# Performance work log

Hardware: AMD Instinct MI355X
Metric: run time of the kernel (lower is better)

Reference implementation:

```python
import jax, jax.numpy as jnp
import numpy as np

N_NODES = 100000


def setup_inputs() -> dict:
    key = jax.random.key(0)
    ks = jax.random.split(key, 8)
    E = 1600000
    x = jax.random.normal(ks[0], (N_NODES, 128), dtype=jnp.float32)
    src = jax.random.randint(ks[1], (E,), 0, N_NODES, dtype=jnp.int32)
    dst = jax.random.randint(ks[2], (E,), 0, N_NODES, dtype=jnp.int32)
    s = 1.0 / np.sqrt(128.0)
    w_self = jax.random.normal(ks[3], (5, 128, 128), dtype=jnp.float32) * s
    w_neigh = jax.random.normal(ks[4], (5, 128, 128), dtype=jnp.float32) * s
    b = jnp.zeros((5, 128), dtype=jnp.float32)
    w_self_out = jax.random.normal(ks[5], (128, 47), dtype=jnp.float32) * s
    w_neigh_out = jax.random.normal(ks[6], (128, 47), dtype=jnp.float32) * s
    b_out = jnp.zeros((47,), dtype=jnp.float32)
    return {"x": x, "src": src, "dst": dst, "w_self": w_self, "w_neigh": w_neigh,
            "b": b, "w_self_out": w_self_out, "w_neigh_out": w_neigh_out, "b_out": b_out}


def _mean_agg(h, src, dst, inv_deg):
    # segment-sum of source features into destination nodes, then mean
    summed = jax.ops.segment_sum(h[src], dst, num_segments=N_NODES)  # [N, d]
    return summed * inv_deg[:, None]


def _sage_layer(h, src, dst, inv_deg, ws, wn, bias):
    neigh = _mean_agg(h, src, dst, inv_deg)
    return h @ ws + neigh @ wn + bias


def reference(x, src, dst, w_self, w_neigh, b, w_self_out, w_neigh_out, b_out):
    # in-degree, clamped to 1 for isolated nodes (DGL mean aggregator behavior)
    deg = jax.ops.segment_sum(jnp.ones_like(dst, dtype=x.dtype), dst, num_segments=N_NODES)
    inv_deg = 1.0 / jnp.maximum(deg, 1.0)

    # layer 0: no ReLU after (matches original forward)
    h = _sage_layer(x, src, dst, inv_deg, w_self[0], w_neigh[0], b[0])
    # layers 1..4: SAGEConv + ReLU
    for i in range(1, 5):
        h = _sage_layer(h, src, dst, inv_deg, w_self[i], w_neigh[i], b[i])
        h = jax.nn.relu(h)
    # final layer: 128 -> num_classes, no activation
    h = _sage_layer(h, src, dst, inv_deg, w_self_out, w_neigh_out, b_out)
    return h
```

## Files before the change

kernel.cpp:

```cpp
#include <hip/hip_runtime.h>

typedef float f4 __attribute__((ext_vector_type(4)));
typedef float f32x4 __attribute__((ext_vector_type(4)));
typedef float f2 __attribute__((ext_vector_type(2)));
typedef short s16x8 __attribute__((ext_vector_type(8)));
typedef int i4 __attribute__((ext_vector_type(4)));

#define N_NODES 100000
#define NBUCK 196
#define NB1 256

__device__ inline unsigned short f2bf(float f) {
    unsigned int u = __builtin_bit_cast(unsigned int, f);
    u += 0x7FFFu + ((u >> 16) & 1u);
    return (unsigned short)(u >> 16);
}
__device__ inline float bflo(unsigned int v) { return __builtin_bit_cast(float, v << 16); }
__device__ inline float bfhi(unsigned int v) { return __builtin_bit_cast(float, v & 0xFFFF0000u); }

#define GLDS(gp, lp)                                                            \
    __builtin_amdgcn_global_load_lds(                                           \
        (const __attribute__((address_space(1))) void*)(gp),                    \
        (__attribute__((address_space(3))) void*)(lp), 16, 0, 0)

__device__ inline void acc8(f2& a0, f2& a1, f2& a2, f2& a3, i4 u) {
    f2 t0 = {bflo((unsigned int)u[0]), bfhi((unsigned int)u[0])};
    f2 t1 = {bflo((unsigned int)u[1]), bfhi((unsigned int)u[1])};
    f2 t2 = {bflo((unsigned int)u[2]), bfhi((unsigned int)u[2])};
    f2 t3 = {bflo((unsigned int)u[3]), bfhi((unsigned int)u[3])};
    a0 += t0; a1 += t1; a2 += t2; a3 += t3;
}


__global__ __launch_bounds__(256) void k_hist(const int* __restrict__ dst,
                                              int* __restrict__ histG, int E) {
    __shared__ int h[NBUCK];
    int tid = threadIdx.x;
    for (int i = tid; i < NBUCK; i += 256) h[i] = 0;
    __syncthreads();
    int chunk = (E + NB1 - 1) / NB1;
    int s = blockIdx.x * chunk, eN = min(E, s + chunk);
    for (int i = s + tid; i < eN; i += 256) atomicAdd(&h[dst[i] >> 9], 1);
    __syncthreads();
    for (int i = tid; i < NBUCK; i += 256) histG[i * NB1 + blockIdx.x] = h[i];
}

__global__ __launch_bounds__(1024) void k_scanB(int* __restrict__ histG) {
    __shared__ int ps[1024];
    int t = threadIdx.x;
    int base = t * 49;
    int vals[49];
    int sum = 0;
#pragma unroll
    for (int i = 0; i < 49; ++i) { vals[i] = histG[base + i]; sum += vals[i]; }
    ps[t] = sum;
    __syncthreads();
    for (int off = 1; off < 1024; off <<= 1) {
        int v = (t >= off) ? ps[t - off] : 0;
        __syncthreads();
        ps[t] += v;
        __syncthreads();
    }
    int run = ps[t] - sum;
#pragma unroll
    for (int i = 0; i < 49; ++i) { int v = vals[i]; histG[base + i] = run; run += v; }
}

__global__ __launch_bounds__(256) void k_place(const int* __restrict__ src,
                                               const int* __restrict__ dst,
                                               const int* __restrict__ histG,
                                               unsigned int* __restrict__ ebuf, int E) {
    __shared__ int cur[NBUCK];
    int tid = threadIdx.x;
    for (int i = tid; i < NBUCK; i += 256) cur[i] = histG[i * NB1 + blockIdx.x];
    __syncthreads();
    int chunk = (E + NB1 - 1) / NB1;
    int s = blockIdx.x * chunk, eN = min(E, s + chunk);
    for (int i = s + tid; i < eN; i += 256) {
        int d = dst[i];
        int b = d >> 9;
        int pos = atomicAdd(&cur[b], 1);
        ebuf[pos] = (unsigned int)src[i] | ((unsigned int)(d & 511) << 17);
    }
}

__global__ __launch_bounds__(256) void k_csr(const unsigned int* __restrict__ ebuf,
                                             const int* __restrict__ histG,
                                             int* __restrict__ rp, int* __restrict__ col,
                                             float* __restrict__ invd, int N, int E) {
    __shared__ int ldeg[512];
    __shared__ int lbase[512];
    int b = blockIdx.x, tid = threadIdx.x;
    int base = histG[b * NB1];
    int endB = (b == NBUCK - 1) ? E : histG[(b + 1) * NB1];
    int cnt = endB - base;
    int n0 = b << 9;

    ldeg[tid] = 0;
    ldeg[tid + 256] = 0;
    __syncthreads();
    for (int i = tid; i < cnt; i += 256) atomicAdd(&ldeg[ebuf[base + i] >> 17], 1);
    __syncthreads();

    int a0 = ldeg[tid], a1 = ldeg[tid + 256];
    lbase[tid] = a0;
    lbase[tid + 256] = a1;
    __syncthreads();
    for (int off = 1; off < 512; off <<= 1) {
        int v0 = (tid >= off) ? lbase[tid - off] : 0;
        int v1 = (tid + 256 >= off) ? lbase[tid + 256 - off] : 0;
        __syncthreads();
        lbase[tid] += v0;
        lbase[tid + 256] += v1;
        __syncthreads();
    }
    int e0 = lbase[tid] - a0, e1 = lbase[tid + 256] - a1;
    __syncthreads();
    lbase[tid] = e0;
    lbase[tid + 256] = e1;
    ldeg[tid] = 0;
    ldeg[tid + 256] = 0;
    __syncthreads();

    for (int i = tid; i < cnt; i += 256) {
        unsigned int p = ebuf[base + i];
        int dl = p >> 17;
        int pos = base + lbase[dl] + atomicAdd(&ldeg[dl], 1);
        col[pos] = (int)(p & 0x1FFFFu) << 8;
    }

    int g0 = n0 + tid, g1 = n0 + tid + 256;
    if (g0 < N) { rp[g0] = base + e0; invd[g0] = 1.0f / fmaxf((float)a0, 1.0f); }
    if (g1 < N) { rp[g1] = base + e1; invd[g1] = 1.0f / fmaxf((float)a1, 1.0f); }
    if (b == NBUCK - 1 && tid == 0) rp[N] = E;
    if (b == NBUCK - 1 && tid < 32) col[E + tid] = 0;
}


__global__ void k_cvt(const float* __restrict__ x, unsigned short* __restrict__ xb, int n8) {
    int t = blockIdx.x * 256 + threadIdx.x;
    if (t >= n8) return;
    f4 a = *(const f4*)&x[(size_t)t * 8];
    f4 b = *(const f4*)&x[(size_t)t * 8 + 4];
    s16x8 p;
    p[0] = (short)f2bf(a[0]); p[1] = (short)f2bf(a[1]);
    p[2] = (short)f2bf(a[2]); p[3] = (short)f2bf(a[3]);
    p[4] = (short)f2bf(b[0]); p[5] = (short)f2bf(b[1]);
    p[6] = (short)f2bf(b[2]); p[7] = (short)f2bf(b[3]);
    *(s16x8*)&xb[(size_t)t * 8] = p;
}

__global__ void k_prepw(const float* __restrict__ ws, const float* __restrict__ wn,
                        unsigned short* __restrict__ wp) {
    int t = blockIdx.x * 256 + threadIdx.x;
    if (t >= 5 * 4096) return;
    int l = t & 63, nfg = (t >> 6) & 7, ks = (t >> 9) & 7, lyr = t >> 12;
    int n = nfg * 16 + (l & 15);
    s16x8 p;
#pragma unroll
    for (int j = 0; j < 8; ++j) {
        int k = ks * 32 + (l >> 4) * 8 + j;
        float v = (k < 128) ? ws[((size_t)lyr * 128 + k) * 128 + n]
                            : wn[((size_t)lyr * 128 + (k - 128)) * 128 + n];
        p[j] = (short)f2bf(v);
    }
    *(s16x8*)&wp[(size_t)t * 8] = p;
}

__global__ void k_prepwo(const float* __restrict__ wso, const float* __restrict__ wno,
                         unsigned short* __restrict__ wS, unsigned short* __restrict__ wN,
                         const float* __restrict__ bo, float* __restrict__ bo48) {
    int t = blockIdx.x * 256 + threadIdx.x;
    if (t < 48) bo48[t] = (t < 47) ? bo[t] : 0.f;
    if (t >= 2 * 768) return;
    int tbl = t / 768, r = t % 768;
    int ks = r / 192, nf = (r / 64) % 3, l = r & 63;
    int n = nf * 16 + (l & 15);
    const float* W = tbl ? wno : wso;
    unsigned short* dstp = tbl ? wN : wS;
    s16x8 p;
#pragma unroll
    for (int j = 0; j < 8; ++j) {
        int k = ks * 32 + (l >> 4) * 8 + j;
        float v = (n < 47) ? W[(size_t)k * 47 + n] : 0.f;
        p[j] = (short)f2bf(v);
    }
    *(s16x8*)&dstp[(size_t)r * 8] = p;
}


__global__ __launch_bounds__(256) void k_agg(const unsigned short* __restrict__ h,
                                             const int* __restrict__ rp,
                                             const int* __restrict__ col,
                                             const float* __restrict__ invd,
                                             unsigned short* __restrict__ out, int n) {
    int gw = (blockIdx.x * 256 + threadIdx.x) >> 6;
    int lane = threadIdx.x & 63;
    if (gw >= n) return;
    const char* hb = (const char*)h;
    const int sub = lane >> 4;
    const int lb = (lane & 15) * 16;
    int beg = rp[gw], end = rp[gw + 1];
    f2 a0 = {0.f, 0.f}, a1 = {0.f, 0.f}, a2 = {0.f, 0.f}, a3 = {0.f, 0.f};
    int e = beg;
    for (; e + 16 <= end; e += 16) {
        unsigned int c0 = (unsigned int)col[e + sub];
        unsigned int c1 = (unsigned int)col[e + 4 + sub];
        unsigned int c2 = (unsigned int)col[e + 8 + sub];
        unsigned int c3 = (unsigned int)col[e + 12 + sub];
        i4 u0, u1, u2, u3;
        __builtin_memcpy(&u0, hb + c0 + lb, 16);
        __builtin_memcpy(&u1, hb + c1 + lb, 16);
        __builtin_memcpy(&u2, hb + c2 + lb, 16);
        __builtin_memcpy(&u3, hb + c3 + lb, 16);
        acc8(a0, a1, a2, a3, u0);
        acc8(a0, a1, a2, a3, u1);
        acc8(a0, a1, a2, a3, u2);
        acc8(a0, a1, a2, a3, u3);
    }
    if (e + 8 <= end) {
        unsigned int c0 = (unsigned int)col[e + sub];
        unsigned int c1 = (unsigned int)col[e + 4 + sub];
        i4 u0, u1;
        __builtin_memcpy(&u0, hb + c0 + lb, 16);
        __builtin_memcpy(&u1, hb + c1 + lb, 16);
        acc8(a0, a1, a2, a3, u0);
        acc8(a0, a1, a2, a3, u1);
        e += 8;
    }
    if (e < end) {
        unsigned int c0 = (unsigned int)col[e + sub];
        unsigned int c1 = (unsigned int)col[e + 4 + sub];
        i4 u0, u1;
        __builtin_memcpy(&u0, hb + c0 + lb, 16);
        __builtin_memcpy(&u1, hb + c1 + lb, 16);
        if (e + sub < end) acc8(a0, a1, a2, a3, u0);
        if (e + 4 + sub < end) acc8(a0, a1, a2, a3, u1);
    }
#pragma unroll
    for (int off = 16; off <= 32; off <<= 1) {
        a0[0] += __shfl_xor(a0[0], off); a0[1] += __shfl_xor(a0[1], off);
        a1[0] += __shfl_xor(a1[0], off); a1[1] += __shfl_xor(a1[1], off);
        a2[0] += __shfl_xor(a2[0], off); a2[1] += __shfl_xor(a2[1], off);
        a3[0] += __shfl_xor(a3[0], off); a3[1] += __shfl_xor(a3[1], off);
    }
    if (lane < 16) {
        float iv = invd[gw];
        i4 r;
        r[0] = (int)((unsigned int)f2bf(a0[0] * iv) | ((unsigned int)f2bf(a0[1] * iv) << 16));
        r[1] = (int)((unsigned int)f2bf(a1[0] * iv) | ((unsigned int)f2bf(a1[1] * iv) << 16));
        r[2] = (int)((unsigned int)f2bf(a2[0] * iv) | ((unsigned int)f2bf(a2[1] * iv) << 16));
        r[3] = (int)((unsigned int)f2bf(a3[0] * iv) | ((unsigned int)f2bf(a3[1] * iv) << 16));
        *(i4*)((char*)out + (size_t)gw * 256 + lb) = r;
    }
}


__global__ __launch_bounds__(256) void gemm128(const unsigned short* __restrict__ h,
                                               const unsigned short* __restrict__ nb,
                                               const unsigned short* __restrict__ wl,
                                               const float* __restrict__ bias,
                                               unsigned short* __restrict__ out,
                                               int M, int relu) {
    __shared__ s16x8 afr[4096];
    const int tid = threadIdx.x;
    const int l = tid & 63, w = tid >> 6;
    const int r0 = blockIdx.x * 128;
    const int cg = (w * 4 + (l >> 4)) * 8;

#pragma unroll
    for (int i = 0; i < 8; ++i) {
        int r = r0 + i * 16 + (l & 15);
        if (r >= M) r = M - 1;
        GLDS(h + (size_t)r * 128 + cg, &afr[(w * 8 + i) * 64]);
        GLDS(nb + (size_t)r * 128 + cg, &afr[((w + 4) * 8 + i) * 64]);
    }
    asm volatile("s_waitcnt vmcnt(0)");
    __syncthreads();

    const int mh = w >> 1, nh = w & 1;
    const s16x8* wf = (const s16x8*)wl;

    f32x4 acc[4][4];
#pragma unroll
    for (int i = 0; i < 4; ++i)
#pragma unroll
        for (int j = 0; j < 4; ++j) acc[i][j] = (f32x4)0.f;

#pragma unroll
    for (int ks = 0; ks < 8; ++ks) {
        s16x8 bw[4], ha[4];
#pragma unroll
        for (int nf = 0; nf < 4; ++nf) bw[nf] = wf[(ks * 8 + nh * 4 + nf) * 64 + l];
#pragma unroll
        for (int mf = 0; mf < 4; ++mf) ha[mf] = afr[(ks * 8 + mh * 4 + mf) * 64 + l];
#pragma unroll
        for (int mf = 0; mf < 4; ++mf)
#pragma unroll
            for (int nf = 0; nf < 4; ++nf)
                acc[mf][nf] = __builtin_amdgcn_mfma_f32_16x16x32_bf16(bw[nf], ha[mf],
                                                                      acc[mf][nf], 0, 0, 0);
    }

    f4 bv[4];
#pragma unroll
    for (int nf = 0; nf < 4; ++nf)
        bv[nf] = *(const f4*)&bias[nh * 64 + nf * 16 + ((l >> 4) << 2)];

#pragma unroll
    for (int mf = 0; mf < 4; ++mf) {
        int row = r0 + mh * 64 + mf * 16 + (l & 15);
        if (row >= M) continue;
#pragma unroll
        for (int nf = 0; nf < 4; ++nf) {
            int ncol = nh * 64 + nf * 16 + ((l >> 4) << 2);
            f32x4 a = acc[mf][nf];
            float v0 = a[0] + bv[nf][0], v1 = a[1] + bv[nf][1];
            float v2 = a[2] + bv[nf][2], v3 = a[3] + bv[nf][3];
            if (relu) {
                v0 = fmaxf(v0, 0.f); v1 = fmaxf(v1, 0.f);
                v2 = fmaxf(v2, 0.f); v3 = fmaxf(v3, 0.f);
            }
            uint2 p;
            p.x = (unsigned int)f2bf(v0) | ((unsigned int)f2bf(v1) << 16);
            p.y = (unsigned int)f2bf(v2) | ((unsigned int)f2bf(v3) << 16);
            *(uint2*)(out + (size_t)row * 128 + ncol) = p;
        }
    }
}


__global__ __launch_bounds__(256) void gemm_fin(const unsigned short* __restrict__ h,
                                                const unsigned short* __restrict__ wS,
                                                const unsigned short* __restrict__ wN,
                                                const float* __restrict__ bo48,
                                                unsigned short* __restrict__ tmpn,
                                                float* __restrict__ selfo, int M) {
    const int tid = threadIdx.x;
    const int l = tid & 63, wv = tid >> 6;
    const int mh = wv >> 1, sel = wv & 1;
    const int r0 = blockIdx.x * 64;
    const s16x8* wf = (const s16x8*)(sel ? wN : wS);
    const int cgb = (l >> 4) << 3;

    int R[2];
#pragma unroll
    for (int mf = 0; mf < 2; ++mf) {
        int r = r0 + mh * 32 + mf * 16 + (l & 15);
        R[mf] = (r > M - 1) ? (M - 1) : r;
    }

    f32x4 acc[2][3];
#pragma unroll
    for (int i = 0; i < 2; ++i)
#pragma unroll
        for (int j = 0; j < 3; ++j) acc[i][j] = (f32x4)0.f;

#pragma unroll
    for (int ks = 0; ks < 4; ++ks) {
        s16x8 ha[2];
#pragma unroll
        for (int mf = 0; mf < 2; ++mf)
            ha[mf] = *(const s16x8*)(h + (size_t)R[mf] * 128 + ks * 32 + cgb);
#pragma unroll
        for (int nf = 0; nf < 3; ++nf) {
            s16x8 bw = wf[(ks * 3 + nf) * 64 + l];
            acc[0][nf] = __builtin_amdgcn_mfma_f32_16x16x32_bf16(bw, ha[0], acc[0][nf], 0, 0, 0);
            acc[1][nf] = __builtin_amdgcn_mfma_f32_16x16x32_bf16(bw, ha[1], acc[1][nf], 0, 0, 0);
        }
    }

#pragma unroll
    for (int mf = 0; mf < 2; ++mf) {
        int row = r0 + mh * 32 + mf * 16 + (l & 15);
        if (row >= M) continue;
#pragma unroll
        for (int nf = 0; nf < 3; ++nf) {
            int ncol = nf * 16 + ((l >> 4) << 2);
            f32x4 a = acc[mf][nf];
            if (sel == 0) {
                f4 bv = *(const f4*)&bo48[ncol];
                f4 o;
                o[0] = a[0] + bv[0]; o[1] = a[1] + bv[1];
                o[2] = a[2] + bv[2]; o[3] = a[3] + bv[3];
                *(f4*)&selfo[(size_t)row * 48 + ncol] = o;
            } else {
                uint2 p;
                p.x = (unsigned int)f2bf(a[0]) | ((unsigned int)f2bf(a[1]) << 16);
                p.y = (unsigned int)f2bf(a[2]) | ((unsigned int)f2bf(a[3]) << 16);
                *(uint2*)(tmpn + (size_t)row * 64 + ncol) = p;
            }
        }
    }
}


__global__ __launch_bounds__(256) void k_agg_fin(const unsigned short* __restrict__ z,
                                                 const float* __restrict__ selfo,
                                                 const int* __restrict__ rp,
                                                 const int* __restrict__ col,
                                                 const float* __restrict__ invd,
                                                 float* __restrict__ out, int n) {
    int gw = (blockIdx.x * 256 + threadIdx.x) >> 6;
    int lane = threadIdx.x & 63;
    if (gw >= n) return;
    const char* zb = (const char*)z;
    const int hhalf = lane >> 5;
    const int lb = (lane & 31) * 4;
    int beg = rp[gw], end = rp[gw + 1];
    f2 acc = {0.f, 0.f};
    int e = beg;
    for (; e + 8 <= end; e += 8) {
        unsigned int u[4];
#pragma unroll
        for (int j = 0; j < 4; ++j) {
            unsigned int c = (unsigned int)col[e + 2 * j + hhalf];
            u[j] = *(const unsigned int*)(zb + (c >> 1) + lb);
        }
#pragma unroll
        for (int j = 0; j < 4; ++j) { f2 v = {bflo(u[j]), bfhi(u[j])}; acc += v; }
    }
    if (e < end) {
        int rem = end - e;
        unsigned int u[4];
#pragma unroll
        for (int j = 0; j < 4; ++j) {
            unsigned int c = (unsigned int)col[e + 2 * j + hhalf];
            u[j] = *(const unsigned int*)(zb + (c >> 1) + lb);
        }
#pragma unroll
        for (int j = 0; j < 4; ++j) {
            if (2 * j + hhalf < rem) { f2 v = {bflo(u[j]), bfhi(u[j])}; acc += v; }
        }
    }
    f2 tot;
    tot[0] = acc[0] + __shfl_xor(acc[0], 32);
    tot[1] = acc[1] + __shfl_xor(acc[1], 32);
    float iv = invd[gw];
    if (lane < 24) {
        int c0 = lane * 2;
        f2 s = *(const f2*)&selfo[(size_t)gw * 48 + c0];
        out[(size_t)gw * 47 + c0] = s[0] + tot[0] * iv;
        if (c0 + 1 < 47) out[(size_t)gw * 47 + c0 + 1] = s[1] + tot[1] * iv;
    }
}


static inline char* alignp(char* p) {
    return (char*)(((size_t)p + 255) & ~(size_t)255);
}

extern "C" void kernel_launch(void* const* d_in, const int* in_sizes, int n_in,
                              void* d_out, int out_size, void* d_ws, size_t ws_size,
                              hipStream_t stream) {
    const float* x = (const float*)d_in[0];
    const int* src = (const int*)d_in[1];
    const int* dst = (const int*)d_in[2];
    const float* w_self = (const float*)d_in[3];
    const float* w_neigh = (const float*)d_in[4];
    const float* b = (const float*)d_in[5];
    const float* wso = (const float*)d_in[6];
    const float* wno = (const float*)d_in[7];
    const float* bo = (const float*)d_in[8];
    float* out = (float*)d_out;

    const int N = N_NODES;
    const int E = in_sizes[1];

    char* w = (char*)d_ws;
    unsigned short* xb = (unsigned short*)w;   w = alignp(w + (size_t)N * 128 * 2);
    unsigned short* hA = (unsigned short*)w;   w = alignp(w + (size_t)N * 128 * 2);
    unsigned short* hB = (unsigned short*)w;   w = alignp(w + (size_t)N * 128 * 2);
    unsigned short* nbuf = (unsigned short*)w; w = alignp(w + (size_t)N * 128 * 2);
    unsigned short* wp = (unsigned short*)w;   w = alignp(w + (size_t)5 * 32768 * 2);
    unsigned short* wS = (unsigned short*)w;   w = alignp(w + (size_t)768 * 8 * 2);
    unsigned short* wN = (unsigned short*)w;   w = alignp(w + (size_t)768 * 8 * 2);
    float* bo48 = (float*)w; w = alignp(w + 48 * 4);
    int* rp = (int*)w;       w = alignp(w + (size_t)(N + 4) * 4);
    int* col = (int*)w;      w = alignp(w + (size_t)(E + 32) * 4);
    int* histG = (int*)w;    w = alignp(w + (size_t)NBUCK * NB1 * 4);
    float* invd = (float*)w; w = alignp(w + (size_t)N * 4);

    unsigned int* ebuf = (unsigned int*)hB;
    unsigned short* tmpn = nbuf;

    k_hist<<<NB1, 256, 0, stream>>>(dst, histG, E);
    k_scanB<<<1, 1024, 0, stream>>>(histG);
    k_place<<<NB1, 256, 0, stream>>>(src, dst, histG, ebuf, E);
    k_csr<<<NBUCK, 256, 0, stream>>>(ebuf, histG, rp, col, invd, N, E);

    k_cvt<<<(N * 128 / 8 + 255) / 256, 256, 0, stream>>>(x, xb, N * 128 / 8);
    k_prepw<<<(5 * 4096 + 255) / 256, 256, 0, stream>>>(w_self, w_neigh, wp);
    k_prepwo<<<6, 256, 0, stream>>>(wso, wno, wS, wN, bo, bo48);

    const int aggBlocks = (N * 64 + 255) / 256;
    const int gemmBlocks = (N + 127) / 128;
    const int finBlocks = (N + 63) / 64;

    k_agg<<<aggBlocks, 256, 0, stream>>>(xb, rp, col, invd, nbuf, N);
    gemm128<<<gemmBlocks, 256, 0, stream>>>(xb, nbuf, wp, b, hA, N, 0);

    unsigned short* cur = hA;
    unsigned short* oth = hB;
    for (int lyr = 1; lyr < 5; ++lyr) {
        k_agg<<<aggBlocks, 256, 0, stream>>>(cur, rp, col, invd, nbuf, N);
        gemm128<<<gemmBlocks, 256, 0, stream>>>(cur, nbuf, wp + (size_t)lyr * 32768,
                                                b + (size_t)lyr * 128, oth, N, 1);
        unsigned short* t = cur; cur = oth; oth = t;
    }

    float* selfo = (float*)hB;
    gemm_fin<<<finBlocks, 256, 0, stream>>>(cur, wS, wN, bo48, tmpn, selfo, N);
    k_agg_fin<<<aggBlocks, 256, 0, stream>>>(tmpn, selfo, rp, col, invd, out, N);
}
```

Measured before the change: 561.4 us.

## Shrink GEMM row tiles to 64, stage final GEMM input via LDS, reduce agg unroll

```diff
diff --git a/kernel.cpp b/kernel.cpp
--- a/kernel.cpp
+++ b/kernel.cpp
@@ -203,39 +203,23 @@
     int beg = rp[gw], end = rp[gw + 1];
     f2 a0 = {0.f, 0.f}, a1 = {0.f, 0.f}, a2 = {0.f, 0.f}, a3 = {0.f, 0.f};
     int e = beg;
-    for (; e + 16 <= end; e += 16) {
+    for (; e + 8 <= end; e += 8) {
         unsigned int c0 = (unsigned int)col[e + sub];
         unsigned int c1 = (unsigned int)col[e + 4 + sub];
-        unsigned int c2 = (unsigned int)col[e + 8 + sub];
-        unsigned int c3 = (unsigned int)col[e + 12 + sub];
-        i4 u0, u1, u2, u3;
-        __builtin_memcpy(&u0, hb + c0 + lb, 16);
-        __builtin_memcpy(&u1, hb + c1 + lb, 16);
-        __builtin_memcpy(&u2, hb + c2 + lb, 16);
-        __builtin_memcpy(&u3, hb + c3 + lb, 16);
-        acc8(a0, a1, a2, a3, u0);
-        acc8(a0, a1, a2, a3, u1);
-        acc8(a0, a1, a2, a3, u2);
-        acc8(a0, a1, a2, a3, u3);
-    }
-    if (e + 8 <= end) {
-        unsigned int c0 = (unsigned int)col[e + sub];
-        unsigned int c1 = (unsigned int)col[e + 4 + sub];
-        i4 u0, u1;
-        __builtin_memcpy(&u0, hb + c0 + lb, 16);
-        __builtin_memcpy(&u1, hb + c1 + lb, 16);
-        acc8(a0, a1, a2, a3, u0);
-        acc8(a0, a1, a2, a3, u1);
-        e += 8;
+        i4 u, v;
+        __builtin_memcpy(&u, hb + c0 + lb, 16);
+        __builtin_memcpy(&v, hb + c1 + lb, 16);
+        acc8(a0, a1, a2, a3, u);
+        acc8(a0, a1, a2, a3, v);
     }
     if (e < end) {
         unsigned int c0 = (unsigned int)col[e + sub];
         unsigned int c1 = (unsigned int)col[e + 4 + sub];
-        i4 u0, u1;
-        __builtin_memcpy(&u0, hb + c0 + lb, 16);
-        __builtin_memcpy(&u1, hb + c1 + lb, 16);
-        if (e + sub < end) acc8(a0, a1, a2, a3, u0);
-        if (e + 4 + sub < end) acc8(a0, a1, a2, a3, u1);
+        i4 u, v;
+        __builtin_memcpy(&u, hb + c0 + lb, 16);
+        __builtin_memcpy(&v, hb + c1 + lb, 16);
+        if (e + sub < end) acc8(a0, a1, a2, a3, u);
+        if (e + 4 + sub < end) acc8(a0, a1, a2, a3, v);
     }
 #pragma unroll
     for (int off = 16; off <= 32; off <<= 1) {
@@ -256,64 +240,64 @@
 }
 
 
-__global__ __launch_bounds__(256) void gemm128(const unsigned short* __restrict__ h,
-                                               const unsigned short* __restrict__ nb,
-                                               const unsigned short* __restrict__ wl,
-                                               const float* __restrict__ bias,
-                                               unsigned short* __restrict__ out,
-                                               int M, int relu) {
-    __shared__ s16x8 afr[4096];
+__global__ __launch_bounds__(256, 4) void gemm128(const unsigned short* __restrict__ h,
+                                                  const unsigned short* __restrict__ nb,
+                                                  const unsigned short* __restrict__ wl,
+                                                  const float* __restrict__ bias,
+                                                  unsigned short* __restrict__ out,
+                                                  int M, int relu) {
+    __shared__ s16x8 afr[2048];
     const int tid = threadIdx.x;
     const int l = tid & 63, w = tid >> 6;
-    const int r0 = blockIdx.x * 128;
+    const int r0 = blockIdx.x * 64;
     const int cg = (w * 4 + (l >> 4)) * 8;
 
 #pragma unroll
-    for (int i = 0; i < 8; ++i) {
+    for (int i = 0; i < 4; ++i) {
         int r = r0 + i * 16 + (l & 15);
         if (r >= M) r = M - 1;
-        GLDS(h + (size_t)r * 128 + cg, &afr[(w * 8 + i) * 64]);
-        GLDS(nb + (size_t)r * 128 + cg, &afr[((w + 4) * 8 + i) * 64]);
+        GLDS(h + (size_t)r * 128 + cg, &afr[(w * 4 + i) * 64]);
+        GLDS(nb + (size_t)r * 128 + cg, &afr[(16 + w * 4 + i) * 64]);
     }
     asm volatile("s_waitcnt vmcnt(0)");
     __syncthreads();
 
-    const int mh = w >> 1, nh = w & 1;
     const s16x8* wf = (const s16x8*)wl;
 
-    f32x4 acc[4][4];
+    f32x4 acc[4][2];
 #pragma unroll
     for (int i = 0; i < 4; ++i)
 #pragma unroll
-        for (int j = 0; j < 4; ++j) acc[i][j] = (f32x4)0.f;
+        for (int j = 0; j < 2; ++j) acc[i][j] = (f32x4)0.f;
 
 #pragma unroll
     for (int ks = 0; ks < 8; ++ks) {
-        s16x8 bw[4], ha[4];
-#pragma unroll
-        for (int nf = 0; nf < 4; ++nf) bw[nf] = wf[(ks * 8 + nh * 4 + nf) * 64 + l];
-#pragma unroll
-        for (int mf = 0; mf < 4; ++mf) ha[mf] = afr[(ks * 8 + mh * 4 + mf) * 64 + l];
+        const int base = (ks < 4) ? (ks * 4) : (16 + (ks - 4) * 4);
+        s16x8 ha[4], bw[2];
+#pragma unroll
+        for (int mf = 0; mf < 4; ++mf) ha[mf] = afr[(base + mf) * 64 + l];
+#pragma unroll
+        for (int nf = 0; nf < 2; ++nf) bw[nf] = wf[(ks * 8 + w * 2 + nf) * 64 + l];
 #pragma unroll
         for (int mf = 0; mf < 4; ++mf)
 #pragma unroll
-            for (int nf = 0; nf < 4; ++nf)
+            for (int nf = 0; nf < 2; ++nf)
                 acc[mf][nf] = __builtin_amdgcn_mfma_f32_16x16x32_bf16(bw[nf], ha[mf],
                                                                       acc[mf][nf], 0, 0, 0);
     }
 
-    f4 bv[4];
-#pragma unroll
-    for (int nf = 0; nf < 4; ++nf)
-        bv[nf] = *(const f4*)&bias[nh * 64 + nf * 16 + ((l >> 4) << 2)];
+    f4 bv[2];
+#pragma unroll
+    for (int nf = 0; nf < 2; ++nf)
+        bv[nf] = *(const f4*)&bias[w * 32 + nf * 16 + ((l >> 4) << 2)];
 
 #pragma unroll
     for (int mf = 0; mf < 4; ++mf) {
-        int row = r0 + mh * 64 + mf * 16 + (l & 15);
+        int row = r0 + mf * 16 + (l & 15);
         if (row >= M) continue;
 #pragma unroll
-        for (int nf = 0; nf < 4; ++nf) {
-            int ncol = nh * 64 + nf * 16 + ((l >> 4) << 2);
+        for (int nf = 0; nf < 2; ++nf) {
+            int ncol = w * 32 + nf * 16 + ((l >> 4) << 2);
             f32x4 a = acc[mf][nf];
             float v0 = a[0] + bv[nf][0], v1 = a[1] + bv[nf][1];
             float v2 = a[2] + bv[nf][2], v3 = a[3] + bv[nf][3];
@@ -330,25 +314,29 @@
 }
 
 
-__global__ __launch_bounds__(256) void gemm_fin(const unsigned short* __restrict__ h,
-                                                const unsigned short* __restrict__ wS,
-                                                const unsigned short* __restrict__ wN,
-                                                const float* __restrict__ bo48,
-                                                unsigned short* __restrict__ tmpn,
-                                                float* __restrict__ selfo, int M) {
+__global__ __launch_bounds__(256, 4) void gemm_fin(const unsigned short* __restrict__ h,
+                                                   const unsigned short* __restrict__ wS,
+                                                   const unsigned short* __restrict__ wN,
+                                                   const float* __restrict__ bo48,
+                                                   unsigned short* __restrict__ tmpn,
+                                                   float* __restrict__ selfo, int M) {
+    __shared__ s16x8 afr[1024];
     const int tid = threadIdx.x;
     const int l = tid & 63, wv = tid >> 6;
+    const int r0 = blockIdx.x * 64;
+    const int cg = (wv * 4 + (l >> 4)) * 8;
+
+#pragma unroll
+    for (int i = 0; i < 4; ++i) {
+        int r = r0 + i * 16 + (l & 15);
+        if (r >= M) r = M - 1;
+        GLDS(h + (size_t)r * 128 + cg, &afr[(wv * 4 + i) * 64]);
+    }
+    asm volatile("s_waitcnt vmcnt(0)");
+    __syncthreads();
+
     const int mh = wv >> 1, sel = wv & 1;
-    const int r0 = blockIdx.x * 64;
     const s16x8* wf = (const s16x8*)(sel ? wN : wS);
-    const int cgb = (l >> 4) << 3;
-
-    int R[2];
-#pragma unroll
-    for (int mf = 0; mf < 2; ++mf) {
-        int r = r0 + mh * 32 + mf * 16 + (l & 15);
-        R[mf] = (r > M - 1) ? (M - 1) : r;
-    }
 
     f32x4 acc[2][3];
 #pragma unroll
@@ -358,16 +346,17 @@
 
 #pragma unroll
     for (int ks = 0; ks < 4; ++ks) {
-        s16x8 ha[2];
+        s16x8 ha[2], bw[3];
+#pragma unroll
+        for (int mf = 0; mf < 2; ++mf) ha[mf] = afr[(ks * 4 + mh * 2 + mf) * 64 + l];
+#pragma unroll
+        for (int nf = 0; nf < 3; ++nf) bw[nf] = wf[(ks * 3 + nf) * 64 + l];
 #pragma unroll
         for (int mf = 0; mf < 2; ++mf)
-            ha[mf] = *(const s16x8*)(h + (size_t)R[mf] * 128 + ks * 32 + cgb);
-#pragma unroll
-        for (int nf = 0; nf < 3; ++nf) {
-            s16x8 bw = wf[(ks * 3 + nf) * 64 + l];
-            acc[0][nf] = __builtin_amdgcn_mfma_f32_16x16x32_bf16(bw, ha[0], acc[0][nf], 0, 0, 0);
-            acc[1][nf] = __builtin_amdgcn_mfma_f32_16x16x32_bf16(bw, ha[1], acc[1][nf], 0, 0, 0);
-        }
+#pragma unroll
+            for (int nf = 0; nf < 3; ++nf)
+                acc[mf][nf] = __builtin_amdgcn_mfma_f32_16x16x32_bf16(bw[nf], ha[mf],
+                                                                      acc[mf][nf], 0, 0, 0);
     }
 
 #pragma unroll
@@ -494,8 +483,7 @@
     k_prepwo<<<6, 256, 0, stream>>>(wso, wno, wS, wN, bo, bo48);
 
     const int aggBlocks = (N * 64 + 255) / 256;
-    const int gemmBlocks = (N + 127) / 128;
-    const int finBlocks = (N + 63) / 64;
+    const int gemmBlocks = (N + 63) / 64;
 
     k_agg<<<aggBlocks, 256, 0, stream>>>(xb, rp, col, invd, nbuf, N);
     gemm128<<<gemmBlocks, 256, 0, stream>>>(xb, nbuf, wp, b, hA, N, 0);
@@ -510,6 +498,6 @@
     }
 
     float* selfo = (float*)hB;
-    gemm_fin<<<finBlocks, 256, 0, stream>>>(cur, wS, wN, bo48, tmpn, selfo, N);
+    gemm_fin<<<gemmBlocks, 256, 0, stream>>>(cur, wS, wN, bo48, tmpn, selfo, N);
     k_agg_fin<<<aggBlocks, 256, 0, stream>>>(tmpn, selfo, rp, col, invd, out, N);
 }
```

Result: no change. 550.8 us (-1.9%).
